# Kernel optimization log

Hardware: AMD Instinct MI355X
Metric: run time of the kernel (lower is better)

The kernel has to match this reference:

```python
import jax, jax.numpy as jnp
import numpy as np

B = 1024          # batch
H = 1024          # rnn_num_hidden
T = 512           # max_length (encoder timesteps)
NUM = 44          # numeric features
EMB = [(30490, 64), (7, 8), (12, 8), (3, 4)]
IN = NUM + sum(d for _, d in EMB)   # input_size = 128


def lstm_cell(x, h, c, w_ih, w_hh, b_ih, b_hh):
    # PyTorch LSTM gate order: i, f, g, o
    g = x @ w_ih.T + h @ w_hh.T + b_ih + b_hh
    i, f, gg, o = jnp.split(g, 4, axis=-1)
    c2 = jax.nn.sigmoid(f) * c + jax.nn.sigmoid(i) * jnp.tanh(gg)
    h2 = jax.nn.sigmoid(o) * jnp.tanh(c2)
    return h2, c2


def setup_inputs():
    key = jax.random.key(0)
    ks = iter(jax.random.split(key, 32))
    nrm = lambda shape, s=0.02: (s * jax.random.normal(next(ks), shape)).astype(jnp.float32)
    return {
        "x": nrm((B, 1, NUM), 1.0),
        "x_emb": jax.random.randint(next(ks), (B, 1, 4), 0, 3),
        "h0": nrm((2, B, H), 1.0),
        "c0": nrm((2, B, H), 1.0),
        "encoder_outputs": nrm((T, B, H), 1.0),
        "emb0": nrm(EMB[0]), "emb1": nrm(EMB[1]), "emb2": nrm(EMB[2]), "emb3": nrm(EMB[3]),
        "attn_w": nrm((T, IN + 2 * H)), "attn_b": nrm((T,)),
        "comb_w": nrm((IN, IN + H)), "comb_b": nrm((IN,)),
        "w_ih0": nrm((4 * H, IN)), "w_hh0": nrm((4 * H, H)),
        "b_ih0": nrm((4 * H,)), "b_hh0": nrm((4 * H,)),
        "w_ih1": nrm((4 * H, H)), "w_hh1": nrm((4 * H, H)),
        "b_ih1": nrm((4 * H,)), "b_hh1": nrm((4 * H,)),
        "pred_w": nrm((1, H)), "pred_b": nrm((1,)),
    }


def reference(x, x_emb, h0, c0, encoder_outputs, emb0, emb1, emb2, emb3,
              attn_w, attn_b, comb_w, comb_b,
              w_ih0, w_hh0, b_ih0, b_hh0, w_ih1, w_hh1, b_ih1, b_hh1,
              pred_w, pred_b):
    xt = x.transpose(1, 0, 2)[0]                       # (B, NUM)
    ids = x_emb.transpose(1, 0, 2)[0]                  # (B, 4)
    e = jnp.concatenate([emb0[ids[:, 0]], emb1[ids[:, 1]],
                         emb2[ids[:, 2]], emb3[ids[:, 3]]], axis=1)
    x_rnn = jnp.concatenate([xt, e], axis=1)           # (B, IN)
    attn_in = jnp.concatenate([x_rnn, h0[0], c0[0]], axis=1)       # (B, IN+2H)
    aw = jax.nn.softmax(attn_in @ attn_w.T + attn_b, axis=1)       # (B, T)
    ctx = jnp.einsum('bt,tbh->bh', aw, encoder_outputs)            # (B, H)
    comb = jnp.concatenate([x_rnn, ctx], axis=1) @ comb_w.T + comb_b  # (B, IN)
    h1, c1 = lstm_cell(comb, h0[0], c0[0], w_ih0, w_hh0, b_ih0, b_hh0)
    h2, c2 = lstm_cell(h1, h0[1], c0[1], w_ih1, w_hh1, b_ih1, b_hh1)
    out = h2 @ pred_w.T + pred_b                       # (B, 1)
    return out, (jnp.stack([h1, h2]), jnp.stack([c1, c2])), aw
```

## Files before the change

### kernel.cpp

```cpp
#include <hip/hip_runtime.h>
#include <hip/hip_bf16.h>

#define B 1024
#define H 1024
#define T 512
#define NUM 44
#define IN 128
#define AK (IN + 2 * H)
#define XC (IN + H)
#define G4 (4 * H)
#define BH ((size_t)B * H)

typedef __attribute__((ext_vector_type(8))) short s16x8;
typedef __attribute__((ext_vector_type(4))) float f32x4;

__device__ __forceinline__ unsigned short f2bf(float f) {
    unsigned u = __float_as_uint(f);
    unsigned r = (u + 0x7fffu + ((u >> 16) & 1u)) >> 16;
    return (unsigned short)r;
}

__device__ __forceinline__ void gload16(const ushort* g, ushort* l) {
    __builtin_amdgcn_global_load_lds(
        (const __attribute__((address_space(1))) void*)g,
        (__attribute__((address_space(3))) void*)l,
        16, 0, 0);
}

#define TM 128
#define TN 128
#define TK 32

__device__ __forceinline__ void gemm_core(
    const ushort* __restrict__ X, const ushort* __restrict__ W,
    const float* __restrict__ bias1, const float* __restrict__ bias2,
    const float* __restrict__ Cin, float* __restrict__ Cf, ushort* __restrict__ Cb,
    int kbeg, int kend, int ldx, int ldw, int ldc,
    int m0, int n0, ushort (*As)[TK], ushort (*Bs)[TK])
{
    const int tid = threadIdx.x;
    const int lane = tid & 63;
    const int wid = tid >> 6;
    const int wm = wid >> 1, wn = wid & 1;
    const int srow = wid * 32 + (lane >> 2);
    const int skc  = (lane & 3) * 8;

    f32x4 acc[4][4] = {};

    for (int k0 = kbeg; k0 < kend; k0 += TK) {
        gload16(X + (size_t)(m0 + srow) * ldx + k0 + skc,      &As[wid * 32][0]);
        gload16(X + (size_t)(m0 + srow + 16) * ldx + k0 + skc, &As[wid * 32 + 16][0]);
        gload16(W + (size_t)(n0 + srow) * ldw + k0 + skc,      &Bs[wid * 32][0]);
        gload16(W + (size_t)(n0 + srow + 16) * ldw + k0 + skc, &Bs[wid * 32 + 16][0]);
        __syncthreads();

        s16x8 a[4], b[4];
        #pragma unroll
        for (int m = 0; m < 4; ++m)
            a[m] = *(const s16x8*)&As[wm * 64 + m * 16 + (lane & 15)][(lane >> 4) * 8];
        #pragma unroll
        for (int n = 0; n < 4; ++n)
            b[n] = *(const s16x8*)&Bs[wn * 64 + n * 16 + (lane & 15)][(lane >> 4) * 8];
        #pragma unroll
        for (int m = 0; m < 4; ++m)
            #pragma unroll
            for (int n = 0; n < 4; ++n)
                acc[m][n] = __builtin_amdgcn_mfma_f32_16x16x32_bf16(a[m], b[n], acc[m][n], 0, 0, 0);
        __syncthreads();
    }

    #pragma unroll
    for (int m = 0; m < 4; ++m) {
        #pragma unroll
        for (int n = 0; n < 4; ++n) {
            int col = n0 + wn * 64 + n * 16 + (lane & 15);
            float badd = (bias1 ? bias1[col] : 0.f) + (bias2 ? bias2[col] : 0.f);
            #pragma unroll
            for (int j = 0; j < 4; ++j) {
                int row = m0 + wm * 64 + m * 16 + (lane >> 4) * 4 + j;
                float v = acc[m][n][j] + badd;
                if (Cin) v += Cin[(size_t)row * ldc + col];
                if (Cf) Cf[(size_t)row * ldc + col] = v;
                if (Cb) Cb[(size_t)row * ldc + col] = f2bf(v);
            }
        }
    }
}

__global__ __launch_bounds__(256) void allgemms_kernel(
    const ushort* __restrict__ attn_in, const ushort* __restrict__ attn_w_bf,
    float* __restrict__ logits_p,
    const ushort* __restrict__ h0_bf,
    const ushort* __restrict__ whh0_bf, const ushort* __restrict__ whh1_bf,
    float* __restrict__ g1buf, float* __restrict__ g2buf,
    const ushort* __restrict__ wih0_bf, const ushort* __restrict__ comb_wT_bf,
    ushort* __restrict__ W_f_bf)
{
    __shared__ ushort As[TM][TK];
    __shared__ ushort Bs[TN][TK];
    const int rid = blockIdx.x;
    if (rid < 128) {
        int z = rid >> 5, t = rid & 31;
        int m0 = (t >> 2) * TM, n0 = (t & 3) * TN;
        gemm_core(attn_in, attn_w_bf, nullptr, nullptr, nullptr,
                  logits_p + (size_t)z * B * T, nullptr,
                  z * 544, z * 544 + 544, AK, AK, T, m0, n0, As, Bs);
    } else if (rid < 640) {
        int layer = (rid - 128) >> 8;
        int t = (rid - 128) & 255;
        int m0 = (t >> 5) * TM, n0 = (t & 31) * TN;
        gemm_core(h0_bf + (size_t)layer * BH, layer ? whh1_bf : whh0_bf,
                  nullptr, nullptr, nullptr, layer ? g2buf : g1buf, nullptr,
                  0, H, H, H, G4, m0, n0, As, Bs);
    } else {
        int t = rid - 640;
        int m0 = (t / 9) * TM, n0 = (t % 9) * TN;
        gemm_core(wih0_bf, comb_wT_bf, nullptr, nullptr, nullptr, nullptr, W_f_bf,
                  0, IN, IN, IN, XC, m0, n0, As, Bs);
    }
}

__global__ __launch_bounds__(256) void gemm64_kernel(
    const ushort* __restrict__ X, const ushort* __restrict__ W,
    const float* __restrict__ bias1, const float* __restrict__ bias2,
    const float* __restrict__ Cin, float* __restrict__ Cf,
    int K, int ldx, int ldw, int ldc)
{
    __shared__ ushort As[64][TK];
    __shared__ ushort Bs[128][TK];
    const int tid = threadIdx.x;
    const int lane = tid & 63;
    const int wid = tid >> 6;
    const int wm = wid >> 1, wn = wid & 1;
    const int m0 = blockIdx.y * 64;
    const int n0 = blockIdx.x * 128;
    const int skc = (lane & 3) * 8;

    f32x4 acc[2][4] = {};

    for (int k0 = 0; k0 < K; k0 += TK) {
        gload16(X + (size_t)(m0 + wid * 16 + (lane >> 2)) * ldx + k0 + skc, &As[wid * 16][0]);
        gload16(W + (size_t)(n0 + wid * 32 + (lane >> 2)) * ldw + k0 + skc, &Bs[wid * 32][0]);
        gload16(W + (size_t)(n0 + wid * 32 + 16 + (lane >> 2)) * ldw + k0 + skc, &Bs[wid * 32 + 16][0]);
        __syncthreads();
        s16x8 a[2], b[4];
        #pragma unroll
        for (int m = 0; m < 2; ++m)
            a[m] = *(const s16x8*)&As[wm * 32 + m * 16 + (lane & 15)][(lane >> 4) * 8];
        #pragma unroll
        for (int n = 0; n < 4; ++n)
            b[n] = *(const s16x8*)&Bs[wn * 64 + n * 16 + (lane & 15)][(lane >> 4) * 8];
        #pragma unroll
        for (int m = 0; m < 2; ++m)
            #pragma unroll
            for (int n = 0; n < 4; ++n)
                acc[m][n] = __builtin_amdgcn_mfma_f32_16x16x32_bf16(a[m], b[n], acc[m][n], 0, 0, 0);
        __syncthreads();
    }

    #pragma unroll
    for (int m = 0; m < 2; ++m) {
        #pragma unroll
        for (int n = 0; n < 4; ++n) {
            int col = n0 + wn * 64 + n * 16 + (lane & 15);
            float badd = (bias1 ? bias1[col] : 0.f) + (bias2 ? bias2[col] : 0.f);
            #pragma unroll
            for (int j = 0; j < 4; ++j) {
                int row = m0 + wm * 32 + m * 16 + (lane >> 4) * 4 + j;
                float v = acc[m][n][j] + badd;
                if (Cin) v += Cin[(size_t)row * ldc + col];
                Cf[(size_t)row * ldc + col] = v;
            }
        }
    }
}

#define P0 2048
#define P1 (P0 + 1088)
#define P2 (P1 + 512)
#define P3 (P2 + 4096)
#define P4 (P3 + 4096)
#define P5 (P4 + 4096)
#define P6 (P5 + 576)
#define P7 (P6 + 16)
#define P8 (P7 + 1024)

__global__ __launch_bounds__(256) void preamble_kernel(
    const float* __restrict__ h0, const float* __restrict__ attn_w,
    const float* __restrict__ w_ih0, const float* __restrict__ w_hh0,
    const float* __restrict__ w_ih1, const float* __restrict__ w_hh1,
    const float* __restrict__ comb_w, const float* __restrict__ comb_b,
    const float* __restrict__ b_ih0, const float* __restrict__ b_hh0,
    const float* __restrict__ x, const int* __restrict__ x_emb,
    const float* __restrict__ c0,
    const float* __restrict__ e0, const float* __restrict__ e1,
    const float* __restrict__ e2, const float* __restrict__ e3,
    ushort* __restrict__ h0_bf, ushort* __restrict__ attn_w_bf,
    ushort* __restrict__ wih0_bf, ushort* __restrict__ whh0_bf,
    ushort* __restrict__ wih1_bf, ushort* __restrict__ whh1_bf,
    ushort* __restrict__ comb_wT, float* __restrict__ biasf,
    ushort* __restrict__ attn_in, ushort* __restrict__ xctx)
{
    const int bid = blockIdx.x;
    const int tid = threadIdx.x;

    if (bid < P5) {
        const float* s; ushort* d; int f;
        if (bid < P0)      { f = bid * 256 + tid;        s = h0;     d = h0_bf; }
        else if (bid < P1) { f = (bid - P0) * 256 + tid; s = attn_w; d = attn_w_bf; }
        else if (bid < P2) { f = (bid - P1) * 256 + tid; s = w_ih0;  d = wih0_bf; }
        else if (bid < P3) { f = (bid - P2) * 256 + tid; s = w_hh0;  d = whh0_bf; }
        else if (bid < P4) { f = (bid - P3) * 256 + tid; s = w_ih1;  d = wih1_bf; }
        else               { f = (bid - P4) * 256 + tid; s = w_hh1;  d = whh1_bf; }
        float4 v = ((const float4*)s)[f];
        ushort4 o = {f2bf(v.x), f2bf(v.y), f2bf(v.z), f2bf(v.w)};
        ((ushort4*)d)[f] = o;
    } else if (bid < P6) {
        int e = (bid - P5) * 256 + tid;
        int j = e >> 7, k = e & 127;
        comb_wT[e] = f2bf(comb_w[(size_t)k * XC + j]);
    } else if (bid < P7) {
        __shared__ float cb[IN];
        for (int i = tid; i < IN; i += 256) cb[i] = comb_b[i];
        __syncthreads();
        int i = (bid - P6) * 256 + tid;
        float s = b_ih0[i] + b_hh0[i];
        const float* row = w_ih0 + (size_t)i * IN;
        #pragma unroll 8
        for (int j = 0; j < IN; ++j) s += row[j] * cb[j];
        biasf[i] = s;
    } else {
        int b = bid - P7;
        int id0 = x_emb[b * 4 + 0];
        int id1 = x_emb[b * 4 + 1];
        int id2 = x_emb[b * 4 + 2];
        int id3 = x_emb[b * 4 + 3];
        ushort* dst = attn_in + (size_t)b * AK;
        for (int j = tid; j < AK; j += 256) {
            float v;
            if (j < 44)        v = x[b * NUM + j];
            else if (j < 108)  v = e0[id0 * 64 + (j - 44)];
            else if (j < 116)  v = e1[id1 * 8 + (j - 108)];
            else if (j < 124)  v = e2[id2 * 8 + (j - 116)];
            else if (j < 128)  v = e3[id3 * 4 + (j - 124)];
            else if (j < 1152) v = h0[b * H + (j - 128)];
            else               v = c0[b * H + (j - 1152)];
            unsigned short bf = f2bf(v);
            dst[j] = bf;
            if (j < IN) xctx[(size_t)b * XC + j] = bf;
        }
    }
}

__global__ __launch_bounds__(256) void ctx_kernel(
    const float* __restrict__ enc, const float* __restrict__ logits_p,
    const float* __restrict__ attn_b, float* __restrict__ aw_out,
    float* __restrict__ ctxp)
{
    const int b = blockIdx.x >> 1;
    const int z = blockIdx.x & 1;
    const int tid = threadIdx.x;
    __shared__ float w[T];
    __shared__ float red[8];

    float v0 = attn_b[tid], v1 = attn_b[tid + 256];
    #pragma unroll
    for (int q = 0; q < 4; ++q) {
        const float* lp = logits_p + (size_t)q * B * T + (size_t)b * T;
        v0 += lp[tid];
        v1 += lp[tid + 256];
    }
    float m = fmaxf(v0, v1);
    #pragma unroll
    for (int off = 32; off > 0; off >>= 1) m = fmaxf(m, __shfl_down(m, off, 64));
    if ((tid & 63) == 0) red[tid >> 6] = m;
    __syncthreads();
    m = fmaxf(fmaxf(red[0], red[1]), fmaxf(red[2], red[3]));
    float e0 = expf(v0 - m), e1 = expf(v1 - m);
    float s = e0 + e1;
    #pragma unroll
    for (int off = 32; off > 0; off >>= 1) s += __shfl_down(s, off, 64);
    if ((tid & 63) == 0) red[4 + (tid >> 6)] = s;
    __syncthreads();
    s = red[4] + red[5] + red[6] + red[7];
    float inv = 1.0f / s;
    float w0 = e0 * inv, w1 = e1 * inv;
    w[tid] = w0;
    w[tid + 256] = w1;
    if (z == 0) {
        aw_out[(size_t)b * T + tid]       = w0;
        aw_out[(size_t)b * T + tid + 256] = w1;
    }
    __syncthreads();

    const float* p = enc + (size_t)(z * 256) * B * H + (size_t)b * H + tid * 4;
    float4 acc = {0.f, 0.f, 0.f, 0.f};
    for (int t0 = 0; t0 < 256; t0 += 16) {
        float4 vv[16];
        #pragma unroll
        for (int u = 0; u < 16; ++u)
            vv[u] = *(const float4*)(p + (size_t)(t0 + u) * B * H);
        #pragma unroll
        for (int u = 0; u < 16; ++u) {
            float sw = w[z * 256 + t0 + u];
            acc.x += sw * vv[u].x; acc.y += sw * vv[u].y;
            acc.z += sw * vv[u].z; acc.w += sw * vv[u].w;
        }
    }
    *(float4*)(ctxp + (size_t)z * BH + (size_t)b * H + tid * 4) = acc;
}

__global__ __launch_bounds__(256) void ctx_reduce_kernel(
    const float* __restrict__ ctxp, ushort* __restrict__ xctx)
{
    int i = blockIdx.x * 256 + threadIdx.x;
    float4 a = ((const float4*)ctxp)[i];
    float4 c = ((const float4*)(ctxp + BH))[i];
    int f = i * 4;
    int b = f >> 10, h = f & 1023;
    ushort4 o = {f2bf(a.x + c.x), f2bf(a.y + c.y), f2bf(a.z + c.z), f2bf(a.w + c.w)};
    *(ushort4*)(xctx + (size_t)b * XC + IN + h) = o;
}

__device__ __forceinline__ float sigmf(float v) { return 1.0f / (1.0f + expf(-v)); }

__global__ __launch_bounds__(256) void lstm_pointwise_kernel(
    const float* __restrict__ g, const float* __restrict__ c_in,
    float* __restrict__ h_out, float* __restrict__ c_out,
    ushort* __restrict__ h_bf)
{
    int idx = blockIdx.x * 256 + threadIdx.x;
    int b = idx >> 10;
    int j = idx & 1023;
    const float* gr = g + (size_t)b * G4;
    float gi = gr[j];
    float gf = gr[j + H];
    float gc = gr[j + 2 * H];
    float go = gr[j + 3 * H];
    float c = sigmf(gf) * c_in[idx] + sigmf(gi) * tanhf(gc);
    float h = sigmf(go) * tanhf(c);
    h_out[idx] = h;
    c_out[idx] = c;
    if (h_bf) h_bf[idx] = f2bf(h);
}

__global__ __launch_bounds__(256) void pred_kernel(
    const float* __restrict__ h2, const float* __restrict__ pw,
    const float* __restrict__ pb, float* __restrict__ out)
{
    int b = blockIdx.x;
    const float* row = h2 + (size_t)b * H;
    float s = 0.f;
    for (int j = threadIdx.x; j < H; j += 256) s += row[j] * pw[j];
    #pragma unroll
    for (int off = 32; off > 0; off >>= 1) s += __shfl_down(s, off, 64);
    __shared__ float sm[4];
    if ((threadIdx.x & 63) == 0) sm[threadIdx.x >> 6] = s;
    __syncthreads();
    if (threadIdx.x == 0) out[b] = sm[0] + sm[1] + sm[2] + sm[3] + pb[0];
}

extern "C" void kernel_launch(void* const* d_in, const int* in_sizes, int n_in,
                              void* d_out, int out_size, void* d_ws, size_t ws_size,
                              hipStream_t stream) {
    (void)in_sizes; (void)n_in; (void)out_size; (void)ws_size;
    const float* x      = (const float*)d_in[0];
    const int*   x_emb  = (const int*)d_in[1];
    const float* h0     = (const float*)d_in[2];
    const float* c0     = (const float*)d_in[3];
    const float* enc    = (const float*)d_in[4];
    const float* emb0   = (const float*)d_in[5];
    const float* emb1   = (const float*)d_in[6];
    const float* emb2   = (const float*)d_in[7];
    const float* emb3   = (const float*)d_in[8];
    const float* attn_w = (const float*)d_in[9];
    const float* attn_b = (const float*)d_in[10];
    const float* comb_w = (const float*)d_in[11];
    const float* comb_b = (const float*)d_in[12];
    const float* w_ih0  = (const float*)d_in[13];
    const float* w_hh0  = (const float*)d_in[14];
    const float* b_ih0  = (const float*)d_in[15];
    const float* b_hh0  = (const float*)d_in[16];
    const float* w_ih1  = (const float*)d_in[17];
    const float* w_hh1  = (const float*)d_in[18];
    const float* b_ih1  = (const float*)d_in[19];
    const float* b_hh1  = (const float*)d_in[20];
    const float* pred_w = (const float*)d_in[21];
    const float* pred_b = (const float*)d_in[22];

    float* out = (float*)d_out;
    float* h1_out = out + 1024;
    float* h2_out = out + 1024 + BH;
    float* c1_out = out + 1024 + 2 * BH;
    float* c2_out = out + 1024 + 3 * BH;
    float* aw_out = out + 1024 + 4 * BH;

    char* w = (char*)d_ws;
    ushort* attn_in_bf = (ushort*)w;  w += (size_t)B * AK * 2;
    ushort* h0_bf      = (ushort*)w;  w += (size_t)2 * BH * 2;
    ushort* attn_w_bf  = (ushort*)w;  w += (size_t)T * AK * 2;
    ushort* wih0_bf    = (ushort*)w;  w += (size_t)G4 * IN * 2;
    ushort* whh0_bf    = (ushort*)w;  w += (size_t)G4 * H * 2;
    ushort* wih1_bf    = (ushort*)w;  w += (size_t)G4 * H * 2;
    ushort* whh1_bf    = (ushort*)w;  w += (size_t)G4 * H * 2;
    ushort* comb_wT_bf = (ushort*)w;  w += (size_t)XC * IN * 2;
    ushort* W_f_bf     = (ushort*)w;  w += (size_t)G4 * XC * 2;
    float*  bias_f     = (float*)w;   w += (size_t)G4 * 4;
    ushort* xctx_bf    = (ushort*)w;  w += (size_t)B * XC * 2;
    ushort* h1_bf      = (ushort*)w;  w += (size_t)BH * 2;
    float*  logits_p   = (float*)w;   w += (size_t)4 * B * T * 4;
    float*  g1buf      = (float*)w;   w += (size_t)B * G4 * 4;
    float*  g2buf      = (float*)w;   w += (size_t)B * G4 * 4;
    float*  ctxp       = (float*)d_ws;

    preamble_kernel<<<P8, 256, 0, stream>>>(
        h0, attn_w, w_ih0, w_hh0, w_ih1, w_hh1, comb_w, comb_b, b_ih0, b_hh0,
        x, x_emb, c0, emb0, emb1, emb2, emb3,
        h0_bf, attn_w_bf, wih0_bf, whh0_bf, wih1_bf, whh1_bf, comb_wT_bf, bias_f,
        attn_in_bf, xctx_bf);

    allgemms_kernel<<<928, 256, 0, stream>>>(
        attn_in_bf, attn_w_bf, logits_p,
        h0_bf, whh0_bf, whh1_bf, g1buf, g2buf,
        wih0_bf, comb_wT_bf, W_f_bf);

    ctx_kernel<<<2048, 256, 0, stream>>>(enc, logits_p, attn_b, aw_out, ctxp);

    ctx_reduce_kernel<<<(int)(BH / 4 / 256), 256, 0, stream>>>(ctxp, xctx_bf);

    gemm64_kernel<<<dim3(G4 / 128, B / 64), 256, 0, stream>>>(
        xctx_bf, W_f_bf, bias_f, nullptr, g1buf, g1buf, XC, XC, XC, G4);

    lstm_pointwise_kernel<<<(int)(BH / 256), 256, 0, stream>>>(g1buf, c0, h1_out, c1_out, h1_bf);

    gemm64_kernel<<<dim3(G4 / 128, B / 64), 256, 0, stream>>>(
        h1_bf, wih1_bf, b_ih1, b_hh1, g2buf, g2buf, H, H, H, G4);

    lstm_pointwise_kernel<<<(int)(BH / 256), 256, 0, stream>>>(g2buf, c0 + BH, h2_out, c2_out, nullptr);

    pred_kernel<<<1024, 256, 0, stream>>>(h2_out, pred_w, pred_b, out);
}
```

Before: 609.6 us.

## Fuse LSTM gate GEMMs with pointwise cell update via gate-interleaved weights

Reorders the LSTM weight rows (and biases) so each group of four consecutive output rows holds the i,f,g,o gates of one hidden unit. Each cell update can then run in the GEMM epilogue of a transposed GEMM. The input and recurrent GEMMs are accumulated in one kernel, so the fp32 gate buffers and the separate pointwise kernels are no longer needed. Softmax is split out of the context kernel, and the context reduction now splits T four ways for more parallelism. This removes several large gate-buffer round trips through memory, at the cost of one more kernel launch, a shared-memory transpose in the epilogue, and recurrent GEMMs that no longer overlap with the attention GEMM.

```diff
diff --git a/kernel.cpp b/kernel.cpp
--- a/kernel.cpp
+++ b/kernel.cpp
@@ -19,6 +19,7 @@
     unsigned r = (u + 0x7fffu + ((u >> 16) & 1u)) >> 16;
     return (unsigned short)r;
 }
+__device__ __forceinline__ float sigmf(float v) { return 1.0f / (1.0f + expf(-v)); }
 
 __device__ __forceinline__ void gload16(const ushort* g, ushort* l) {
     __builtin_amdgcn_global_load_lds(
@@ -33,8 +34,7 @@
 
 __device__ __forceinline__ void gemm_core(
     const ushort* __restrict__ X, const ushort* __restrict__ W,
-    const float* __restrict__ bias1, const float* __restrict__ bias2,
-    const float* __restrict__ Cin, float* __restrict__ Cf, ushort* __restrict__ Cb,
+    float* __restrict__ Cf, ushort* __restrict__ Cb, int permrow,
     int kbeg, int kend, int ldx, int ldw, int ldc,
     int m0, int n0, ushort (*As)[TK], ushort (*Bs)[TK])
 {
@@ -74,14 +74,15 @@
         #pragma unroll
         for (int n = 0; n < 4; ++n) {
             int col = n0 + wn * 64 + n * 16 + (lane & 15);
-            float badd = (bias1 ? bias1[col] : 0.f) + (bias2 ? bias2[col] : 0.f);
             #pragma unroll
             for (int j = 0; j < 4; ++j) {
                 int row = m0 + wm * 64 + m * 16 + (lane >> 4) * 4 + j;
-                float v = acc[m][n][j] + badd;
-                if (Cin) v += Cin[(size_t)row * ldc + col];
+                float v = acc[m][n][j];
                 if (Cf) Cf[(size_t)row * ldc + col] = v;
-                if (Cb) Cb[(size_t)row * ldc + col] = f2bf(v);
+                if (Cb) {
+                    int r = permrow ? (((row & 1023) << 2) | (row >> 10)) : row;
+                    Cb[(size_t)r * ldc + col] = f2bf(v);
+                }
             }
         }
     }
@@ -90,9 +91,6 @@
 __global__ __launch_bounds__(256) void allgemms_kernel(
     const ushort* __restrict__ attn_in, const ushort* __restrict__ attn_w_bf,
     float* __restrict__ logits_p,
-    const ushort* __restrict__ h0_bf,
-    const ushort* __restrict__ whh0_bf, const ushort* __restrict__ whh1_bf,
-    float* __restrict__ g1buf, float* __restrict__ g2buf,
     const ushort* __restrict__ wih0_bf, const ushort* __restrict__ comb_wT_bf,
     ushort* __restrict__ W_f_bf)
 {
@@ -102,75 +100,114 @@
     if (rid < 128) {
         int z = rid >> 5, t = rid & 31;
         int m0 = (t >> 2) * TM, n0 = (t & 3) * TN;
-        gemm_core(attn_in, attn_w_bf, nullptr, nullptr, nullptr,
-                  logits_p + (size_t)z * B * T, nullptr,
+        gemm_core(attn_in, attn_w_bf, logits_p + (size_t)z * B * T, nullptr, 0,
                   z * 544, z * 544 + 544, AK, AK, T, m0, n0, As, Bs);
-    } else if (rid < 640) {
-        int layer = (rid - 128) >> 8;
-        int t = (rid - 128) & 255;
-        int m0 = (t >> 5) * TM, n0 = (t & 31) * TN;
-        gemm_core(h0_bf + (size_t)layer * BH, layer ? whh1_bf : whh0_bf,
-                  nullptr, nullptr, nullptr, layer ? g2buf : g1buf, nullptr,
-                  0, H, H, H, G4, m0, n0, As, Bs);
     } else {
-        int t = rid - 640;
+        int t = rid - 128;
         int m0 = (t / 9) * TM, n0 = (t % 9) * TN;
-        gemm_core(wih0_bf, comb_wT_bf, nullptr, nullptr, nullptr, nullptr, W_f_bf,
+        gemm_core(wih0_bf, comb_wT_bf, nullptr, W_f_bf, 1,
                   0, IN, IN, IN, XC, m0, n0, As, Bs);
     }
 }
 
-__global__ __launch_bounds__(256) void gemm64_kernel(
-    const ushort* __restrict__ X, const ushort* __restrict__ W,
-    const float* __restrict__ bias1, const float* __restrict__ bias2,
-    const float* __restrict__ Cin, float* __restrict__ Cf,
-    int K, int ldx, int ldw, int ldc)
-{
-    __shared__ ushort As[64][TK];
-    __shared__ ushort Bs[128][TK];
+__global__ __launch_bounds__(256) void gemm_lstm_T_kernel(
+    const ushort* __restrict__ W1, const ushort* __restrict__ X1, int K1,
+    const ushort* __restrict__ W2, const ushort* __restrict__ X2, int K2,
+    const float* __restrict__ biasp,
+    const float* __restrict__ c_in, float* __restrict__ h_out, float* __restrict__ c_out,
+    ushort* __restrict__ h_bf)
+{
+    __shared__ union {
+        struct { ushort As[128][TK]; ushort Bs[64][TK]; } g;
+        float e[2][64][33];
+    } sh;
+
     const int tid = threadIdx.x;
     const int lane = tid & 63;
     const int wid = tid >> 6;
     const int wm = wid >> 1, wn = wid & 1;
-    const int m0 = blockIdx.y * 64;
-    const int n0 = blockIdx.x * 128;
+    const int m0 = blockIdx.y * 128;
+    const int n0 = blockIdx.x * 64;
     const int skc = (lane & 3) * 8;
-
-    f32x4 acc[2][4] = {};
-
-    for (int k0 = 0; k0 < K; k0 += TK) {
-        gload16(X + (size_t)(m0 + wid * 16 + (lane >> 2)) * ldx + k0 + skc, &As[wid * 16][0]);
-        gload16(W + (size_t)(n0 + wid * 32 + (lane >> 2)) * ldw + k0 + skc, &Bs[wid * 32][0]);
-        gload16(W + (size_t)(n0 + wid * 32 + 16 + (lane >> 2)) * ldw + k0 + skc, &Bs[wid * 32 + 16][0]);
-        __syncthreads();
-        s16x8 a[2], b[4];
-        #pragma unroll
-        for (int m = 0; m < 2; ++m)
-            a[m] = *(const s16x8*)&As[wm * 32 + m * 16 + (lane & 15)][(lane >> 4) * 8];
-        #pragma unroll
-        for (int n = 0; n < 4; ++n)
-            b[n] = *(const s16x8*)&Bs[wn * 64 + n * 16 + (lane & 15)][(lane >> 4) * 8];
-        #pragma unroll
-        for (int m = 0; m < 2; ++m)
+    const int srow = wid * 32 + (lane >> 2);
+
+    f32x4 acc[4][2] = {};
+
+    #pragma unroll
+    for (int phase = 0; phase < 2; ++phase) {
+        const ushort* Wp = phase ? W2 : W1;
+        const ushort* Xp = phase ? X2 : X1;
+        const int K = phase ? K2 : K1;
+        for (int k0 = 0; k0 < K; k0 += TK) {
+            gload16(Wp + (size_t)(m0 + srow) * K + k0 + skc,      &sh.g.As[wid * 32][0]);
+            gload16(Wp + (size_t)(m0 + srow + 16) * K + k0 + skc, &sh.g.As[wid * 32 + 16][0]);
+            gload16(Xp + (size_t)(n0 + wid * 16 + (lane >> 2)) * K + k0 + skc, &sh.g.Bs[wid * 16][0]);
+            __syncthreads();
+            s16x8 a[4], b[2];
             #pragma unroll
-            for (int n = 0; n < 4; ++n)
-                acc[m][n] = __builtin_amdgcn_mfma_f32_16x16x32_bf16(a[m], b[n], acc[m][n], 0, 0, 0);
-        __syncthreads();
-    }
-
-    #pragma unroll
-    for (int m = 0; m < 2; ++m) {
-        #pragma unroll
-        for (int n = 0; n < 4; ++n) {
-            int col = n0 + wn * 64 + n * 16 + (lane & 15);
-            float badd = (bias1 ? bias1[col] : 0.f) + (bias2 ? bias2[col] : 0.f);
+            for (int m = 0; m < 4; ++m)
+                a[m] = *(const s16x8*)&sh.g.As[wm * 64 + m * 16 + (lane & 15)][(lane >> 4) * 8];
             #pragma unroll
-            for (int j = 0; j < 4; ++j) {
-                int row = m0 + wm * 32 + m * 16 + (lane >> 4) * 4 + j;
-                float v = acc[m][n][j] + badd;
-                if (Cin) v += Cin[(size_t)row * ldc + col];
-                Cf[(size_t)row * ldc + col] = v;
-            }
+            for (int n = 0; n < 2; ++n)
+                b[n] = *(const s16x8*)&sh.g.Bs[wn * 32 + n * 16 + (lane & 15)][(lane >> 4) * 8];
+            #pragma unroll
+            for (int m = 0; m < 4; ++m)
+                #pragma unroll
+                for (int n = 0; n < 2; ++n)
+                    acc[m][n] = __builtin_amdgcn_mfma_f32_16x16x32_bf16(a[m], b[n], acc[m][n], 0, 0, 0);
+            __syncthreads();
+        }
+    }
+
+    const int ubase = m0 >> 2;
+    {
+        int col = tid >> 2, u0 = (tid & 3) * 8;
+        const float* src = c_in + (size_t)(n0 + col) * H + ubase + u0;
+        float4 v0 = *(const float4*)src;
+        float4 v1 = *(const float4*)(src + 4);
+        sh.e[0][col][u0 + 0] = v0.x; sh.e[0][col][u0 + 1] = v0.y;
+        sh.e[0][col][u0 + 2] = v0.z; sh.e[0][col][u0 + 3] = v0.w;
+        sh.e[0][col][u0 + 4] = v1.x; sh.e[0][col][u0 + 5] = v1.y;
+        sh.e[0][col][u0 + 6] = v1.z; sh.e[0][col][u0 + 7] = v1.w;
+    }
+    __syncthreads();
+
+    #pragma unroll
+    for (int m = 0; m < 4; ++m) {
+        #pragma unroll
+        for (int n = 0; n < 2; ++n) {
+            int row0 = m0 + wm * 64 + m * 16 + (lane >> 4) * 4;
+            int u_local = (wm * 64 + m * 16 + (lane >> 4) * 4) >> 2;
+            int col_local = wn * 32 + n * 16 + (lane & 15);
+            float4 bb = ((const float4*)biasp)[row0 >> 2];
+            float gi = acc[m][n][0] + bb.x;
+            float gf = acc[m][n][1] + bb.y;
+            float gg = acc[m][n][2] + bb.z;
+            float go = acc[m][n][3] + bb.w;
+            float cprev = sh.e[0][col_local][u_local];
+            float c = sigmf(gf) * cprev + sigmf(gi) * tanhf(gg);
+            float h = sigmf(go) * tanhf(c);
+            sh.e[0][col_local][u_local] = c;
+            sh.e[1][col_local][u_local] = h;
+        }
+    }
+    __syncthreads();
+
+    {
+        int col = tid >> 2, u0 = (tid & 3) * 8;
+        size_t base = (size_t)(n0 + col) * H + ubase + u0;
+        float cb[8], hb[8];
+        #pragma unroll
+        for (int u = 0; u < 8; ++u) { cb[u] = sh.e[0][col][u0 + u]; hb[u] = sh.e[1][col][u0 + u]; }
+        *(float4*)(c_out + base)     = make_float4(cb[0], cb[1], cb[2], cb[3]);
+        *(float4*)(c_out + base + 4) = make_float4(cb[4], cb[5], cb[6], cb[7]);
+        *(float4*)(h_out + base)     = make_float4(hb[0], hb[1], hb[2], hb[3]);
+        *(float4*)(h_out + base + 4) = make_float4(hb[4], hb[5], hb[6], hb[7]);
+        if (h_bf) {
+            ushort4 o0 = {f2bf(hb[0]), f2bf(hb[1]), f2bf(hb[2]), f2bf(hb[3])};
+            ushort4 o1 = {f2bf(hb[4]), f2bf(hb[5]), f2bf(hb[6]), f2bf(hb[7])};
+            *(ushort4*)(h_bf + base) = o0;
+            *(ushort4*)(h_bf + base + 4) = o1;
         }
     }
 }
@@ -183,7 +220,8 @@
 #define P5 (P4 + 4096)
 #define P6 (P5 + 576)
 #define P7 (P6 + 16)
-#define P8 (P7 + 1024)
+#define P8 (P7 + 16)
+#define P9 (P8 + 1024)
 
 __global__ __launch_bounds__(256) void preamble_kernel(
     const float* __restrict__ h0, const float* __restrict__ attn_w,
@@ -191,28 +229,36 @@
     const float* __restrict__ w_ih1, const float* __restrict__ w_hh1,
     const float* __restrict__ comb_w, const float* __restrict__ comb_b,
     const float* __restrict__ b_ih0, const float* __restrict__ b_hh0,
+    const float* __restrict__ b_ih1, const float* __restrict__ b_hh1,
     const float* __restrict__ x, const int* __restrict__ x_emb,
     const float* __restrict__ c0,
     const float* __restrict__ e0, const float* __restrict__ e1,
     const float* __restrict__ e2, const float* __restrict__ e3,
     ushort* __restrict__ h0_bf, ushort* __restrict__ attn_w_bf,
-    ushort* __restrict__ wih0_bf, ushort* __restrict__ whh0_bf,
-    ushort* __restrict__ wih1_bf, ushort* __restrict__ whh1_bf,
-    ushort* __restrict__ comb_wT, float* __restrict__ biasf,
+    ushort* __restrict__ wih0_bf, ushort* __restrict__ whh0p,
+    ushort* __restrict__ wih1p, ushort* __restrict__ whh1p,
+    ushort* __restrict__ comb_wT, float* __restrict__ biasf, float* __restrict__ bias2p,
     ushort* __restrict__ attn_in, ushort* __restrict__ xctx)
 {
     const int bid = blockIdx.x;
     const int tid = threadIdx.x;
 
-    if (bid < P5) {
+    if (bid < P2) {
         const float* s; ushort* d; int f;
         if (bid < P0)      { f = bid * 256 + tid;        s = h0;     d = h0_bf; }
         else if (bid < P1) { f = (bid - P0) * 256 + tid; s = attn_w; d = attn_w_bf; }
-        else if (bid < P2) { f = (bid - P1) * 256 + tid; s = w_ih0;  d = wih0_bf; }
-        else if (bid < P3) { f = (bid - P2) * 256 + tid; s = w_hh0;  d = whh0_bf; }
-        else if (bid < P4) { f = (bid - P3) * 256 + tid; s = w_ih1;  d = wih1_bf; }
-        else               { f = (bid - P4) * 256 + tid; s = w_hh1;  d = whh1_bf; }
+        else               { f = (bid - P1) * 256 + tid; s = w_ih0;  d = wih0_bf; }
         float4 v = ((const float4*)s)[f];
+        ushort4 o = {f2bf(v.x), f2bf(v.y), f2bf(v.z), f2bf(v.w)};
+        ((ushort4*)d)[f] = o;
+    } else if (bid < P5) {
+        const float* s; ushort* d; int f;
+        if (bid < P3)      { f = (bid - P2) * 256 + tid; s = w_hh0; d = whh0p; }
+        else if (bid < P4) { f = (bid - P3) * 256 + tid; s = w_ih1; d = wih1p; }
+        else               { f = (bid - P4) * 256 + tid; s = w_hh1; d = whh1p; }
+        int r = f >> 8, c = f & 255;
+        int srcrow = ((r & 3) << 10) + (r >> 2);
+        float4 v = ((const float4*)s)[srcrow * 256 + c];
         ushort4 o = {f2bf(v.x), f2bf(v.y), f2bf(v.z), f2bf(v.w)};
         ((ushort4*)d)[f] = o;
     } else if (bid < P6) {
@@ -223,14 +269,19 @@
         __shared__ float cb[IN];
         for (int i = tid; i < IN; i += 256) cb[i] = comb_b[i];
         __syncthreads();
-        int i = (bid - P6) * 256 + tid;
-        float s = b_ih0[i] + b_hh0[i];
-        const float* row = w_ih0 + (size_t)i * IN;
+        int p = (bid - P6) * 256 + tid;
+        int srow = ((p & 3) << 10) + (p >> 2);
+        float s = b_ih0[srow] + b_hh0[srow];
+        const float* row = w_ih0 + (size_t)srow * IN;
         #pragma unroll 8
         for (int j = 0; j < IN; ++j) s += row[j] * cb[j];
-        biasf[i] = s;
+        biasf[p] = s;
+    } else if (bid < P8) {
+        int p = (bid - P7) * 256 + tid;
+        int srow = ((p & 3) << 10) + (p >> 2);
+        bias2p[p] = b_ih1[srow] + b_hh1[srow];
     } else {
-        int b = bid - P7;
+        int b = bid - P8;
         int id0 = x_emb[b * 4 + 0];
         int id1 = x_emb[b * 4 + 1];
         int id2 = x_emb[b * 4 + 2];
@@ -252,21 +303,17 @@
     }
 }
 
-__global__ __launch_bounds__(256) void ctx_kernel(
-    const float* __restrict__ enc, const float* __restrict__ logits_p,
-    const float* __restrict__ attn_b, float* __restrict__ aw_out,
-    float* __restrict__ ctxp)
-{
-    const int b = blockIdx.x >> 1;
-    const int z = blockIdx.x & 1;
-    const int tid = threadIdx.x;
-    __shared__ float w[T];
+__global__ __launch_bounds__(256) void softmax_kernel(
+    const float* __restrict__ logits_p, const float* __restrict__ attn_b,
+    float* __restrict__ aw)
+{
+    int b = blockIdx.x;
+    int tid = threadIdx.x;
     __shared__ float red[8];
-
     float v0 = attn_b[tid], v1 = attn_b[tid + 256];
     #pragma unroll
-    for (int q = 0; q < 4; ++q) {
-        const float* lp = logits_p + (size_t)q * B * T + (size_t)b * T;
+    for (int z = 0; z < 4; ++z) {
+        const float* lp = logits_p + (size_t)z * B * T + (size_t)b * T;
         v0 += lp[tid];
         v1 += lp[tid + 256];
     }
@@ -284,25 +331,31 @@
     __syncthreads();
     s = red[4] + red[5] + red[6] + red[7];
     float inv = 1.0f / s;
-    float w0 = e0 * inv, w1 = e1 * inv;
-    w[tid] = w0;
-    w[tid + 256] = w1;
-    if (z == 0) {
-        aw_out[(size_t)b * T + tid]       = w0;
-        aw_out[(size_t)b * T + tid + 256] = w1;
-    }
-    __syncthreads();
-
-    const float* p = enc + (size_t)(z * 256) * B * H + (size_t)b * H + tid * 4;
+    aw[(size_t)b * T + tid]       = v0 = e0 * inv;
+    aw[(size_t)b * T + tid + 256] = e1 * inv;
+}
+
+__global__ __launch_bounds__(256) void ctx_kernel(
+    const float* __restrict__ enc, const float* __restrict__ aw,
+    float* __restrict__ ctxp)
+{
+    const int b = blockIdx.x >> 2;
+    const int z = blockIdx.x & 3;
+    const int tid = threadIdx.x;
+    __shared__ float w[128];
+    if (tid < 128) w[tid] = aw[(size_t)b * T + z * 128 + tid];
+    __syncthreads();
+
+    const float* p = enc + (size_t)(z * 128) * BH + (size_t)b * H + tid * 4;
     float4 acc = {0.f, 0.f, 0.f, 0.f};
-    for (int t0 = 0; t0 < 256; t0 += 16) {
+    for (int t0 = 0; t0 < 128; t0 += 16) {
         float4 vv[16];
         #pragma unroll
         for (int u = 0; u < 16; ++u)
-            vv[u] = *(const float4*)(p + (size_t)(t0 + u) * B * H);
+            vv[u] = *(const float4*)(p + (size_t)(t0 + u) * BH);
         #pragma unroll
         for (int u = 0; u < 16; ++u) {
-            float sw = w[z * 256 + t0 + u];
+            float sw = w[t0 + u];
             acc.x += sw * vv[u].x; acc.y += sw * vv[u].y;
             acc.z += sw * vv[u].z; acc.w += sw * vv[u].w;
         }
@@ -315,33 +368,14 @@
 {
     int i = blockIdx.x * 256 + threadIdx.x;
     float4 a = ((const float4*)ctxp)[i];
-    float4 c = ((const float4*)(ctxp + BH))[i];
+    float4 b4 = ((const float4*)(ctxp + BH))[i];
+    float4 c = ((const float4*)(ctxp + 2 * BH))[i];
+    float4 d = ((const float4*)(ctxp + 3 * BH))[i];
     int f = i * 4;
     int b = f >> 10, h = f & 1023;
-    ushort4 o = {f2bf(a.x + c.x), f2bf(a.y + c.y), f2bf(a.z + c.z), f2bf(a.w + c.w)};
+    ushort4 o = {f2bf(a.x + b4.x + c.x + d.x), f2bf(a.y + b4.y + c.y + d.y),
+                 f2bf(a.z + b4.z + c.z + d.z), f2bf(a.w + b4.w + c.w + d.w)};
     *(ushort4*)(xctx + (size_t)b * XC + IN + h) = o;
-}
-
-__device__ __forceinline__ float sigmf(float v) { return 1.0f / (1.0f + expf(-v)); }
-
-__global__ __launch_bounds__(256) void lstm_pointwise_kernel(
-    const float* __restrict__ g, const float* __restrict__ c_in,
-    float* __restrict__ h_out, float* __restrict__ c_out,
-    ushort* __restrict__ h_bf)
-{
-    int idx = blockIdx.x * 256 + threadIdx.x;
-    int b = idx >> 10;
-    int j = idx & 1023;
-    const float* gr = g + (size_t)b * G4;
-    float gi = gr[j];
-    float gf = gr[j + H];
-    float gc = gr[j + 2 * H];
-    float go = gr[j + 3 * H];
-    float c = sigmf(gf) * c_in[idx] + sigmf(gi) * tanhf(gc);
-    float h = sigmf(go) * tanhf(c);
-    h_out[idx] = h;
-    c_out[idx] = c;
-    if (h_bf) h_bf[idx] = f2bf(h);
 }
 
 __global__ __launch_bounds__(256) void pred_kernel(
@@ -400,43 +434,41 @@
     ushort* h0_bf      = (ushort*)w;  w += (size_t)2 * BH * 2;
     ushort* attn_w_bf  = (ushort*)w;  w += (size_t)T * AK * 2;
     ushort* wih0_bf    = (ushort*)w;  w += (size_t)G4 * IN * 2;
-    ushort* whh0_bf    = (ushort*)w;  w += (size_t)G4 * H * 2;
-    ushort* wih1_bf    = (ushort*)w;  w += (size_t)G4 * H * 2;
-    ushort* whh1_bf    = (ushort*)w;  w += (size_t)G4 * H * 2;
+    ushort* whh0p      = (ushort*)w;  w += (size_t)G4 * H * 2;
+    ushort* wih1p      = (ushort*)w;  w += (size_t)G4 * H * 2;
+    ushort* whh1p      = (ushort*)w;  w += (size_t)G4 * H * 2;
     ushort* comb_wT_bf = (ushort*)w;  w += (size_t)XC * IN * 2;
     ushort* W_f_bf     = (ushort*)w;  w += (size_t)G4 * XC * 2;
     float*  bias_f     = (float*)w;   w += (size_t)G4 * 4;
+    float*  bias2p     = (float*)w;   w += (size_t)G4 * 4;
     ushort* xctx_bf    = (ushort*)w;  w += (size_t)B * XC * 2;
     ushort* h1_bf      = (ushort*)w;  w += (size_t)BH * 2;
     float*  logits_p   = (float*)w;   w += (size_t)4 * B * T * 4;
-    float*  g1buf      = (float*)w;   w += (size_t)B * G4 * 4;
-    float*  g2buf      = (float*)w;   w += (size_t)B * G4 * 4;
-    float*  ctxp       = (float*)d_ws;
-
-    preamble_kernel<<<P8, 256, 0, stream>>>(
-        h0, attn_w, w_ih0, w_hh0, w_ih1, w_hh1, comb_w, comb_b, b_ih0, b_hh0,
+    float*  ctxp       = (float*)w;   w += (size_t)4 * BH * 4;
+
+    preamble_kernel<<<P9, 256, 0, stream>>>(
+        h0, attn_w, w_ih0, w_hh0, w_ih1, w_hh1, comb_w, comb_b,
+        b_ih0, b_hh0, b_ih1, b_hh1,
         x, x_emb, c0, emb0, emb1, emb2, emb3,
-        h0_bf, attn_w_bf, wih0_bf, whh0_bf, wih1_bf, whh1_bf, comb_wT_bf, bias_f,
-        attn_in_bf, xctx_bf);
-
-    allgemms_kernel<<<928, 256, 0, stream>>>(
-        attn_in_bf, attn_w_bf, logits_p,
-        h0_bf, whh0_bf, whh1_bf, g1buf, g2buf,
-        wih0_bf, comb_wT_bf, W_f_bf);
-
-    ctx_kernel<<<2048, 256, 0, stream>>>(enc, logits_p, attn_b, aw_out, ctxp);
+        h0_bf, attn_w_bf, wih0_bf, whh0p, wih1p, whh1p, comb_wT_bf,
+        bias_f, bias2p, attn_in_bf, xctx_bf);
+
+    allgemms_kernel<<<416, 256, 0, stream>>>(
+        attn_in_bf, attn_w_bf, logits_p, wih0_bf, comb_wT_bf, W_f_bf);
+
+    softmax_kernel<<<B, 256, 0, stream>>>(logits_p, attn_b, aw_out);
+
+    ctx_kernel<<<4096, 256, 0, stream>>>(enc, aw_out, ctxp);
 
     ctx_reduce_kernel<<<(int)(BH / 4 / 256), 256, 0, stream>>>(ctxp, xctx_bf);
 
-    gemm64_kernel<<<dim3(G4 / 128, B / 64), 256, 0, stream>>>(
-        xctx_bf, W_f_bf, bias_f, nullptr, g1buf, g1buf, XC, XC, XC, G4);
-
-    lstm_pointwise_kernel<<<(int)(BH / 256), 256, 0, stream>>>(g1buf, c0, h1_out, c1_out, h1_bf);
-
-    gemm64_kernel<<<dim3(G4 / 128, B / 64), 256, 0, stream>>>(
-        h1_bf, wih1_bf, b_ih1, b_hh1, g2buf, g2buf, H, H, H, G4);
-
-    lstm_pointwise_kernel<<<(int)(BH / 256), 256, 0, stream>>>(g2buf, c0 + BH, h2_out, c2_out, nullptr);
-
-    pred_kernel<<<1024, 256, 0, stream>>>(h2_out, pred_w, pred_b, out);
-}
+    gemm_lstm_T_kernel<<<dim3(B / 64, G4 / 128), 256, 0, stream>>>(
+        W_f_bf, xctx_bf, XC, whh0p, h0_bf, H, bias_f,
+        c0, h1_out, c1_out, h1_bf);
+
+    gemm_lstm_T_kernel<<<dim3(B / 64, G4 / 128), 256, 0, stream>>>(
+        wih1p, h1_bf, H, whh1p, h0_bf + BH, H, bias2p,
+        c0 + BH, h2_out, c2_out, nullptr);
+
+    pred_kernel<<<B, 256, 0, stream>>>(h2_out, pred_w, pred_b, out);
+}
```

After: 701.3 us. 15.0% more time.

## Store LSTM gate partials in bf16, split softmax from ctx, vectorize pointwise

Applied to the files above, without the earlier changes.

The recurrent-gate GEMM partials (g1/g2) are now stored as bf16 instead of fp32, which halves the write and read traffic of those B×4H buffers in the GEMMs and the pointwise kernels. Softmax moves into its own kernel so the ctx kernel no longer recomputes it in both of its blocks per row. The ctx unroll depth drops from 16 to 8, and the LSTM pointwise kernel is vectorized to 4 elements per thread. ctxp gets its own workspace region instead of aliasing the start of the workspace. Rounding the gate pre-activations to bf16 adds precision loss, and the extra launch adds a little overhead.

```diff
diff --git a/kernel.cpp b/kernel.cpp
--- a/kernel.cpp
+++ b/kernel.cpp
@@ -19,6 +19,10 @@
     unsigned r = (u + 0x7fffu + ((u >> 16) & 1u)) >> 16;
     return (unsigned short)r;
 }
+__device__ __forceinline__ float bf2f(unsigned short u) {
+    return __uint_as_float(((unsigned)u) << 16);
+}
+__device__ __forceinline__ float sigmf(float v) { return 1.0f / (1.0f + expf(-v)); }
 
 __device__ __forceinline__ void gload16(const ushort* g, ushort* l) {
     __builtin_amdgcn_global_load_lds(
@@ -33,8 +37,7 @@
 
 __device__ __forceinline__ void gemm_core(
     const ushort* __restrict__ X, const ushort* __restrict__ W,
-    const float* __restrict__ bias1, const float* __restrict__ bias2,
-    const float* __restrict__ Cin, float* __restrict__ Cf, ushort* __restrict__ Cb,
+    float* __restrict__ Cf, ushort* __restrict__ Cb,
     int kbeg, int kend, int ldx, int ldw, int ldc,
     int m0, int n0, ushort (*As)[TK], ushort (*Bs)[TK])
 {
@@ -74,12 +77,10 @@
         #pragma unroll
         for (int n = 0; n < 4; ++n) {
             int col = n0 + wn * 64 + n * 16 + (lane & 15);
-            float badd = (bias1 ? bias1[col] : 0.f) + (bias2 ? bias2[col] : 0.f);
             #pragma unroll
             for (int j = 0; j < 4; ++j) {
                 int row = m0 + wm * 64 + m * 16 + (lane >> 4) * 4 + j;
-                float v = acc[m][n][j] + badd;
-                if (Cin) v += Cin[(size_t)row * ldc + col];
+                float v = acc[m][n][j];
                 if (Cf) Cf[(size_t)row * ldc + col] = v;
                 if (Cb) Cb[(size_t)row * ldc + col] = f2bf(v);
             }
@@ -92,7 +93,7 @@
     float* __restrict__ logits_p,
     const ushort* __restrict__ h0_bf,
     const ushort* __restrict__ whh0_bf, const ushort* __restrict__ whh1_bf,
-    float* __restrict__ g1buf, float* __restrict__ g2buf,
+    ushort* __restrict__ g1part, ushort* __restrict__ g2part,
     const ushort* __restrict__ wih0_bf, const ushort* __restrict__ comb_wT_bf,
     ushort* __restrict__ W_f_bf)
 {
@@ -102,20 +103,19 @@
     if (rid < 128) {
         int z = rid >> 5, t = rid & 31;
         int m0 = (t >> 2) * TM, n0 = (t & 3) * TN;
-        gemm_core(attn_in, attn_w_bf, nullptr, nullptr, nullptr,
-                  logits_p + (size_t)z * B * T, nullptr,
+        gemm_core(attn_in, attn_w_bf, logits_p + (size_t)z * B * T, nullptr,
                   z * 544, z * 544 + 544, AK, AK, T, m0, n0, As, Bs);
     } else if (rid < 640) {
         int layer = (rid - 128) >> 8;
         int t = (rid - 128) & 255;
         int m0 = (t >> 5) * TM, n0 = (t & 31) * TN;
         gemm_core(h0_bf + (size_t)layer * BH, layer ? whh1_bf : whh0_bf,
-                  nullptr, nullptr, nullptr, layer ? g2buf : g1buf, nullptr,
+                  nullptr, layer ? g2part : g1part,
                   0, H, H, H, G4, m0, n0, As, Bs);
     } else {
         int t = rid - 640;
         int m0 = (t / 9) * TM, n0 = (t % 9) * TN;
-        gemm_core(wih0_bf, comb_wT_bf, nullptr, nullptr, nullptr, nullptr, W_f_bf,
+        gemm_core(wih0_bf, comb_wT_bf, nullptr, W_f_bf,
                   0, IN, IN, IN, XC, m0, n0, As, Bs);
     }
 }
@@ -123,7 +123,7 @@
 __global__ __launch_bounds__(256) void gemm64_kernel(
     const ushort* __restrict__ X, const ushort* __restrict__ W,
     const float* __restrict__ bias1, const float* __restrict__ bias2,
-    const float* __restrict__ Cin, float* __restrict__ Cf,
+    const ushort* __restrict__ CinBf, ushort* __restrict__ Cb,
     int K, int ldx, int ldw, int ldc)
 {
     __shared__ ushort As[64][TK];
@@ -167,9 +167,8 @@
             #pragma unroll
             for (int j = 0; j < 4; ++j) {
                 int row = m0 + wm * 32 + m * 16 + (lane >> 4) * 4 + j;
-                float v = acc[m][n][j] + badd;
-                if (Cin) v += Cin[(size_t)row * ldc + col];
-                Cf[(size_t)row * ldc + col] = v;
+                float v = acc[m][n][j] + badd + bf2f(CinBf[(size_t)row * ldc + col]);
+                Cb[(size_t)row * ldc + col] = f2bf(v);
             }
         }
     }
@@ -252,21 +251,17 @@
     }
 }
 
-__global__ __launch_bounds__(256) void ctx_kernel(
-    const float* __restrict__ enc, const float* __restrict__ logits_p,
-    const float* __restrict__ attn_b, float* __restrict__ aw_out,
-    float* __restrict__ ctxp)
-{
-    const int b = blockIdx.x >> 1;
-    const int z = blockIdx.x & 1;
-    const int tid = threadIdx.x;
-    __shared__ float w[T];
+__global__ __launch_bounds__(256) void softmax_kernel(
+    const float* __restrict__ logits_p, const float* __restrict__ attn_b,
+    float* __restrict__ aw)
+{
+    int b = blockIdx.x;
+    int tid = threadIdx.x;
     __shared__ float red[8];
-
     float v0 = attn_b[tid], v1 = attn_b[tid + 256];
     #pragma unroll
-    for (int q = 0; q < 4; ++q) {
-        const float* lp = logits_p + (size_t)q * B * T + (size_t)b * T;
+    for (int z = 0; z < 4; ++z) {
+        const float* lp = logits_p + (size_t)z * B * T + (size_t)b * T;
         v0 += lp[tid];
         v1 += lp[tid + 256];
     }
@@ -284,25 +279,31 @@
     __syncthreads();
     s = red[4] + red[5] + red[6] + red[7];
     float inv = 1.0f / s;
-    float w0 = e0 * inv, w1 = e1 * inv;
-    w[tid] = w0;
-    w[tid + 256] = w1;
-    if (z == 0) {
-        aw_out[(size_t)b * T + tid]       = w0;
-        aw_out[(size_t)b * T + tid + 256] = w1;
-    }
+    aw[(size_t)b * T + tid]       = e0 * inv;
+    aw[(size_t)b * T + tid + 256] = e1 * inv;
+}
+
+__global__ __launch_bounds__(256) void ctx_kernel(
+    const float* __restrict__ enc, const float* __restrict__ aw,
+    float* __restrict__ ctxp)
+{
+    const int b = blockIdx.x >> 1;
+    const int z = blockIdx.x & 1;
+    const int tid = threadIdx.x;
+    __shared__ float w[256];
+    w[tid] = aw[(size_t)b * T + z * 256 + tid];
     __syncthreads();
 
-    const float* p = enc + (size_t)(z * 256) * B * H + (size_t)b * H + tid * 4;
+    const float* p = enc + (size_t)(z * 256) * BH + (size_t)b * H + tid * 4;
     float4 acc = {0.f, 0.f, 0.f, 0.f};
-    for (int t0 = 0; t0 < 256; t0 += 16) {
-        float4 vv[16];
-        #pragma unroll
-        for (int u = 0; u < 16; ++u)
-            vv[u] = *(const float4*)(p + (size_t)(t0 + u) * B * H);
-        #pragma unroll
-        for (int u = 0; u < 16; ++u) {
-            float sw = w[z * 256 + t0 + u];
+    for (int t0 = 0; t0 < 256; t0 += 8) {
+        float4 vv[8];
+        #pragma unroll
+        for (int u = 0; u < 8; ++u)
+            vv[u] = *(const float4*)(p + (size_t)(t0 + u) * BH);
+        #pragma unroll
+        for (int u = 0; u < 8; ++u) {
+            float sw = w[t0 + u];
             acc.x += sw * vv[u].x; acc.y += sw * vv[u].y;
             acc.z += sw * vv[u].z; acc.w += sw * vv[u].w;
         }
@@ -322,26 +323,37 @@
     *(ushort4*)(xctx + (size_t)b * XC + IN + h) = o;
 }
 
-__device__ __forceinline__ float sigmf(float v) { return 1.0f / (1.0f + expf(-v)); }
-
 __global__ __launch_bounds__(256) void lstm_pointwise_kernel(
-    const float* __restrict__ g, const float* __restrict__ c_in,
+    const ushort* __restrict__ g, const float* __restrict__ c_in,
     float* __restrict__ h_out, float* __restrict__ c_out,
     ushort* __restrict__ h_bf)
 {
-    int idx = blockIdx.x * 256 + threadIdx.x;
-    int b = idx >> 10;
-    int j = idx & 1023;
-    const float* gr = g + (size_t)b * G4;
-    float gi = gr[j];
-    float gf = gr[j + H];
-    float gc = gr[j + 2 * H];
-    float go = gr[j + 3 * H];
-    float c = sigmf(gf) * c_in[idx] + sigmf(gi) * tanhf(gc);
-    float h = sigmf(go) * tanhf(c);
-    h_out[idx] = h;
-    c_out[idx] = c;
-    if (h_bf) h_bf[idx] = f2bf(h);
+    int q = blockIdx.x * 256 + threadIdx.x;
+    int b = q >> 8;
+    int j = (q & 255) * 4;
+    const ushort* gr = g + (size_t)b * G4 + j;
+    ushort4 gi4 = *(const ushort4*)(gr);
+    ushort4 gf4 = *(const ushort4*)(gr + H);
+    ushort4 gc4 = *(const ushort4*)(gr + 2 * H);
+    ushort4 go4 = *(const ushort4*)(gr + 3 * H);
+    size_t base = (size_t)b * H + j;
+    float4 cin = *(const float4*)(c_in + base);
+    float4 cv, hv;
+    {
+        float c0v = sigmf(bf2f(gf4.x)) * cin.x + sigmf(bf2f(gi4.x)) * tanhf(bf2f(gc4.x));
+        float c1v = sigmf(bf2f(gf4.y)) * cin.y + sigmf(bf2f(gi4.y)) * tanhf(bf2f(gc4.y));
+        float c2v = sigmf(bf2f(gf4.z)) * cin.z + sigmf(bf2f(gi4.z)) * tanhf(bf2f(gc4.z));
+        float c3v = sigmf(bf2f(gf4.w)) * cin.w + sigmf(bf2f(gi4.w)) * tanhf(bf2f(gc4.w));
+        cv = make_float4(c0v, c1v, c2v, c3v);
+        hv = make_float4(sigmf(bf2f(go4.x)) * tanhf(c0v), sigmf(bf2f(go4.y)) * tanhf(c1v),
+                         sigmf(bf2f(go4.z)) * tanhf(c2v), sigmf(bf2f(go4.w)) * tanhf(c3v));
+    }
+    *(float4*)(c_out + base) = cv;
+    *(float4*)(h_out + base) = hv;
+    if (h_bf) {
+        ushort4 o = {f2bf(hv.x), f2bf(hv.y), f2bf(hv.z), f2bf(hv.w)};
+        *(ushort4*)(h_bf + base) = o;
+    }
 }
 
 __global__ __launch_bounds__(256) void pred_kernel(
@@ -408,10 +420,10 @@
     float*  bias_f     = (float*)w;   w += (size_t)G4 * 4;
     ushort* xctx_bf    = (ushort*)w;  w += (size_t)B * XC * 2;
     ushort* h1_bf      = (ushort*)w;  w += (size_t)BH * 2;
+    ushort* g1part     = (ushort*)w;  w += (size_t)B * G4 * 2;
+    ushort* g2part     = (ushort*)w;  w += (size_t)B * G4 * 2;
     float*  logits_p   = (float*)w;   w += (size_t)4 * B * T * 4;
-    float*  g1buf      = (float*)w;   w += (size_t)B * G4 * 4;
-    float*  g2buf      = (float*)w;   w += (size_t)B * G4 * 4;
-    float*  ctxp       = (float*)d_ws;
+    float*  ctxp       = (float*)w;   w += (size_t)2 * BH * 4;
 
     preamble_kernel<<<P8, 256, 0, stream>>>(
         h0, attn_w, w_ih0, w_hh0, w_ih1, w_hh1, comb_w, comb_b, b_ih0, b_hh0,
@@ -421,22 +433,24 @@
 
     allgemms_kernel<<<928, 256, 0, stream>>>(
         attn_in_bf, attn_w_bf, logits_p,
-        h0_bf, whh0_bf, whh1_bf, g1buf, g2buf,
+        h0_bf, whh0_bf, whh1_bf, g1part, g2part,
         wih0_bf, comb_wT_bf, W_f_bf);
 
-    ctx_kernel<<<2048, 256, 0, stream>>>(enc, logits_p, attn_b, aw_out, ctxp);
+    softmax_kernel<<<B, 256, 0, stream>>>(logits_p, attn_b, aw_out);
+
+    ctx_kernel<<<2048, 256, 0, stream>>>(enc, aw_out, ctxp);
 
     ctx_reduce_kernel<<<(int)(BH / 4 / 256), 256, 0, stream>>>(ctxp, xctx_bf);
 
     gemm64_kernel<<<dim3(G4 / 128, B / 64), 256, 0, stream>>>(
-        xctx_bf, W_f_bf, bias_f, nullptr, g1buf, g1buf, XC, XC, XC, G4);
-
-    lstm_pointwise_kernel<<<(int)(BH / 256), 256, 0, stream>>>(g1buf, c0, h1_out, c1_out, h1_bf);
+        xctx_bf, W_f_bf, bias_f, nullptr, g1part, g1part, XC, XC, XC, G4);
+
+    lstm_pointwise_kernel<<<(int)(BH / 4 / 256), 256, 0, stream>>>(g1part, c0, h1_out, c1_out, h1_bf);
 
     gemm64_kernel<<<dim3(G4 / 128, B / 64), 256, 0, stream>>>(
-        h1_bf, wih1_bf, b_ih1, b_hh1, g2buf, g2buf, H, H, H, G4);
-
-    lstm_pointwise_kernel<<<(int)(BH / 256), 256, 0, stream>>>(g2buf, c0 + BH, h2_out, c2_out, nullptr);
-
-    pred_kernel<<<1024, 256, 0, stream>>>(h2_out, pred_w, pred_b, out);
-}
+        h1_bf, wih1_bf, b_ih1, b_hh1, g2part, g2part, H, H, H, G4);
+
+    lstm_pointwise_kernel<<<(int)(BH / 4 / 256), 256, 0, stream>>>(g2part, c0 + BH, h2_out, c2_out, nullptr);
+
+    pred_kernel<<<B, 256, 0, stream>>>(h2_out, pred_w, pred_b, out);
+}
```

New measurement: 590.6 us. 1.03x faster.
